# Kernel tuning notes

Hardware: AMD Instinct MI355X
Metric: run time of the kernel (lower is better)

## Reference

```python
import jax, jax.numpy as jnp
import numpy as np

KERNEL_MUL = 2.0
KERNEL_NUM = 5


def setup_inputs() -> dict:
    key = jax.random.key(0)
    k1, k2 = jax.random.split(key)
    source = jax.random.normal(k1, (4096, 256), dtype=jnp.float32)
    target = jax.random.normal(k2, (4096, 256), dtype=jnp.float32)
    return {"source": source, "target": target}


def _mmd(source, target):
    b = source.shape[0]
    total = jnp.concatenate([source, target], axis=0)  # [2N, D]
    n = total.shape[0]
    # pairwise squared L2 via gram trick (avoids O(N^2 * D) intermediate)
    sq = jnp.sum(total * total, axis=1)  # [2N]
    d2 = sq[:, None] + sq[None, :] - 2.0 * (total @ total.T)
    d2 = jnp.maximum(d2, 0.0)  # [2N, 2N]
    # bandwidth from detached distances (matches L2_distance.data)
    bandwidth = jax.lax.stop_gradient(jnp.sum(d2)) / (n * n - n)
    bandwidth = bandwidth / (KERNEL_MUL ** (KERNEL_NUM // 2))
    kernels = jnp.zeros_like(d2)
    for i in range(KERNEL_NUM):
        kernels = kernels + jnp.exp(-d2 / (bandwidth * KERNEL_MUL ** i))
    XX = kernels[:b, :b]
    YY = kernels[b:, b:]
    XY = kernels[:b, b:]
    YX = kernels[b:, :b]
    return jnp.mean(XX + YY - XY - YX)


def reference(source, target):
    return _mmd(source, target)
```

## Files before the change

kernel.cpp:

```cpp
#include <hip/hip_runtime.h>
#include <hip/hip_bf16.h>


#define N_TOTAL 8192
#define B_HALF 4096
#define D_DIM 256
#define TILE 128
#define NTILE 64
#define NTRI 2080

typedef float f32x16 __attribute__((ext_vector_type(16)));
typedef _Float16 f16x8 __attribute__((ext_vector_type(8)));

__device__ __forceinline__ const float* row_base(const float* src, const float* tgt, int r) {
    return (r < B_HALF) ? src + (size_t)r * D_DIM : tgt + (size_t)(r - B_HALF) * D_DIM;
}

__global__ __launch_bounds__(256) void prep_kernel(const float* __restrict__ src,
                                                   const float* __restrict__ tgt,
                                                   _Float16* __restrict__ a16f,
                                                   float* __restrict__ sq,
                                                   float* __restrict__ colpart) {
    int tid = threadIdx.x, w = tid >> 6, lane = tid & 63;
    int r0 = blockIdx.x * 128;
    #pragma unroll 4
    for (int i = 0; i < 32; ++i) {
        int row = r0 + w * 32 + i;
        const float* rp = row_base(src, tgt, row);
        float4 v = ((const float4*)rp)[lane];
        _Float16 h[4] = {(_Float16)v.x, (_Float16)v.y, (_Float16)v.z, (_Float16)v.w};
        size_t idx = ((size_t)(lane >> 1) * N_TOTAL + row) * 8 + (lane & 1) * 4;
        *(ushort4*)(a16f + idx) = *(ushort4*)h;
        float s = v.x*v.x + v.y*v.y + v.z*v.z + v.w*v.w;
        #pragma unroll
        for (int off = 32; off; off >>= 1) s += __shfl_down(s, off, 64);
        if (lane == 0) sq[row] = s;
    }
    float c = 0.f;
    for (int r = r0; r < r0 + 128; ++r)
        c += row_base(src, tgt, r)[tid];
    colpart[blockIdx.x * D_DIM + tid] = c;
}

__global__ __launch_bounds__(256) void bw_kernel(const float* __restrict__ sq,
                                                 const float* __restrict__ colpart,
                                                 float* __restrict__ negc,
                                                 double* __restrict__ accum) {
    __shared__ double red[256];
    int t = threadIdx.x;
    double s = 0.0;
    for (int i = t; i < N_TOTAL; i += 256) s += (double)sq[i];
    red[t] = s;
    __syncthreads();
    for (int off = 128; off; off >>= 1) {
        if (t < off) red[t] += red[t + off];
        __syncthreads();
    }
    double sumsq = red[0];
    __syncthreads();
    float c = 0.f;
    #pragma unroll
    for (int k = 0; k < 64; ++k) c += colpart[k * D_DIM + t];
    red[t] = (double)c * (double)c;
    __syncthreads();
    for (int off = 128; off; off >>= 1) {
        if (t < off) red[t] += red[t + off];
        __syncthreads();
    }
    if (t == 0) {
        double S1 = 2.0 * (double)N_TOTAL * sumsq - 2.0 * red[0];
        double nn = (double)N_TOTAL * (double)N_TOTAL - (double)N_TOTAL;
        double bw = S1 / nn / 4.0;
        negc[0] = (float)(-1.4426950408889634 / (16.0 * bw));
        accum[0] = 0.0;
    }
}

__global__ __launch_bounds__(256, 4) void mmd_main(const _Float16* __restrict__ a16f,
                                                   const float* __restrict__ sq,
                                                   const float* __restrict__ negc,
                                                   double* __restrict__ accum) {
    __shared__ float wsum[4];

    int b  = blockIdx.x;
    int bs = (b & 7) * (NTRI / 8) + (b >> 3);
    int it = 0, cum = 0;
    while (cum + (NTILE - it) <= bs) { cum += NTILE - it; ++it; }
    int jt = it + (bs - cum);

    int tid = threadIdx.x, lane = tid & 63, wid = tid >> 6;
    int wrow = wid >> 1, wcol = wid & 1;
    int rowA = it * TILE, rowB = jt * TILE;
    int c32 = lane & 31, khalf = lane >> 5;

    const _Float16* PA = a16f + (size_t)khalf * (N_TOTAL * 8)
                              + (size_t)(rowA + wrow * 64 + c32) * 8;
    const _Float16* PB = a16f + (size_t)khalf * (N_TOTAL * 8)
                              + (size_t)(rowB + wcol * 64 + c32) * 8;

    f32x16 acc[2][2] = {};

    #pragma unroll 4
    for (int kap = 0; kap < 16; ++kap) {
        size_t ko = (size_t)kap * (N_TOTAL * 16);
        f16x8 af[2], bf[2];
        af[0] = *(const f16x8*)(PA + ko);
        af[1] = *(const f16x8*)(PA + ko + 32 * 8);
        bf[0] = *(const f16x8*)(PB + ko);
        bf[1] = *(const f16x8*)(PB + ko + 32 * 8);
        #pragma unroll
        for (int mt = 0; mt < 2; ++mt)
            #pragma unroll
            for (int nt = 0; nt < 2; ++nt)
                acc[mt][nt] = __builtin_amdgcn_mfma_f32_32x32x16_f16(af[mt], bf[nt], acc[mt][nt], 0, 0, 0);
    }

    float nc = *negc;
    float sjn[2];
    #pragma unroll
    for (int nt = 0; nt < 2; ++nt)
        sjn[nt] = sq[rowB + wcol * 64 + nt * 32 + c32];
    float tsum = 0.f;
    #pragma unroll
    for (int mt = 0; mt < 2; ++mt) {
        #pragma unroll
        for (int reg = 0; reg < 16; ++reg) {
            int i = rowA + wrow * 64 + mt * 32 + (reg & 3) + 8 * (reg >> 2) + 4 * khalf;
            float si = sq[i];
            #pragma unroll
            for (int nt = 0; nt < 2; ++nt) {
                float d2 = fmaxf(si + sjn[nt] - 2.0f * acc[mt][nt][reg], 0.f);
                float u  = exp2f(nc * d2);
                float u2 = u * u, u4 = u2 * u2, u8 = u4 * u4;
                tsum += u + u2 + u4 + u8 + u8 * u8;
            }
        }
    }
    float scale = (((it < 32) == (jt < 32)) ? 1.f : -1.f) * ((it == jt) ? 1.f : 2.f);
    tsum *= scale;

    #pragma unroll
    for (int off = 32; off; off >>= 1) tsum += __shfl_down(tsum, off, 64);
    if (lane == 0) wsum[wid] = tsum;
    __syncthreads();
    if (tid == 0) {
        float t = wsum[0] + wsum[1] + wsum[2] + wsum[3];
        atomicAdd(accum, (double)t);
    }
}

__global__ void finalize_kernel(const double* __restrict__ accum, float* __restrict__ out) {
    out[0] = (float)(accum[0] / ((double)B_HALF * (double)B_HALF));
}

extern "C" void kernel_launch(void* const* d_in, const int* in_sizes, int n_in,
                              void* d_out, int out_size, void* d_ws, size_t ws_size,
                              hipStream_t stream) {
    const float* src = (const float*)d_in[0];
    const float* tgt = (const float*)d_in[1];
    float* out = (float*)d_out;

    char* ws = (char*)d_ws;
    float*  sq      = (float*)ws;
    float*  colpart = (float*)(ws + 32768);
    float*  negc    = (float*)(ws + 98304);
    double* accum   = (double*)(ws + 98312);
    _Float16* a16f  = (_Float16*)(ws + 131072);

    prep_kernel<<<64, 256, 0, stream>>>(src, tgt, a16f, sq, colpart);
    bw_kernel<<<1, 256, 0, stream>>>(sq, colpart, negc, accum);
    mmd_main<<<NTRI, 256, 0, stream>>>(a16f, sq, negc, accum);
    finalize_kernel<<<1, 1, 0, stream>>>(accum, out);
}
```

Measured before the change: 79.11 us.

## Stage A tile in LDS via direct global-to-LDS loads; widen prep kernel

```diff
diff --git a/kernel.cpp b/kernel.cpp
--- a/kernel.cpp
+++ b/kernel.cpp
@@ -22,24 +22,37 @@
                                                    float* __restrict__ sq,
                                                    float* __restrict__ colpart) {
     int tid = threadIdx.x, w = tid >> 6, lane = tid & 63;
-    int r0 = blockIdx.x * 128;
-    #pragma unroll 4
-    for (int i = 0; i < 32; ++i) {
-        int row = r0 + w * 32 + i;
+    int r0 = blockIdx.x * 32;
+
+    #pragma unroll
+    for (int i = 0; i < 8; ++i) {
+        int row = r0 + w * 8 + i;
         const float* rp = row_base(src, tgt, row);
         float4 v = ((const float4*)rp)[lane];
-        _Float16 h[4] = {(_Float16)v.x, (_Float16)v.y, (_Float16)v.z, (_Float16)v.w};
-        size_t idx = ((size_t)(lane >> 1) * N_TOTAL + row) * 8 + (lane & 1) * 4;
-        *(ushort4*)(a16f + idx) = *(ushort4*)h;
         float s = v.x*v.x + v.y*v.y + v.z*v.z + v.w*v.w;
         #pragma unroll
         for (int off = 32; off; off >>= 1) s += __shfl_down(s, off, 64);
         if (lane == 0) sq[row] = s;
     }
+
     float c = 0.f;
-    for (int r = r0; r < r0 + 128; ++r)
+    for (int r = r0; r < r0 + 32; ++r)
         c += row_base(src, tgt, r)[tid];
     colpart[blockIdx.x * D_DIM + tid] = c;
+
+    int wg = blockIdx.x * 4 + w;
+    #pragma unroll
+    for (int i = 0; i < 4; ++i) {
+        int t  = wg * 4 + i;
+        int kb = t >> 7, rg = t & 127;
+        int row = rg * 64 + lane;
+        const float* rp = row_base(src, tgt, row) + kb * 8;
+        float4 v0 = ((const float4*)rp)[0];
+        float4 v1 = ((const float4*)rp)[1];
+        _Float16 h[8] = {(_Float16)v0.x, (_Float16)v0.y, (_Float16)v0.z, (_Float16)v0.w,
+                         (_Float16)v1.x, (_Float16)v1.y, (_Float16)v1.z, (_Float16)v1.w};
+        *(f16x8*)(a16f + ((size_t)kb * N_TOTAL + row) * 8) = *(f16x8*)h;
+    }
 }
 
 __global__ __launch_bounds__(256) void bw_kernel(const float* __restrict__ sq,
@@ -59,8 +72,7 @@
     double sumsq = red[0];
     __syncthreads();
     float c = 0.f;
-    #pragma unroll
-    for (int k = 0; k < 64; ++k) c += colpart[k * D_DIM + t];
+    for (int k = 0; k < 256; ++k) c += colpart[k * D_DIM + t];
     red[t] = (double)c * (double)c;
     __syncthreads();
     for (int off = 128; off; off >>= 1) {
@@ -76,10 +88,17 @@
     }
 }
 
-__global__ __launch_bounds__(256, 4) void mmd_main(const _Float16* __restrict__ a16f,
+__device__ __forceinline__ void gload_lds16(const void* g, void* l) {
+    __builtin_amdgcn_global_load_lds((const __attribute__((address_space(1))) unsigned int*)g,
+                                     (__attribute__((address_space(3))) unsigned int*)l,
+                                     16, 0, 0);
+}
+
+__global__ __launch_bounds__(256, 2) void mmd_main(const _Float16* __restrict__ a16f,
                                                    const float* __restrict__ sq,
                                                    const float* __restrict__ negc,
                                                    double* __restrict__ accum) {
+    __shared__ _Float16 Asm[32 * TILE * 8];
     __shared__ float wsum[4];
 
     int b  = blockIdx.x;
@@ -93,19 +112,30 @@
     int rowA = it * TILE, rowB = jt * TILE;
     int c32 = lane & 31, khalf = lane >> 5;
 
-    const _Float16* PA = a16f + (size_t)khalf * (N_TOTAL * 8)
-                              + (size_t)(rowA + wrow * 64 + c32) * 8;
+    #pragma unroll
+    for (int i = 0; i < 16; ++i) {
+        int g0 = i * 256 + wid * 64;
+        int g  = g0 + lane;
+        int kb = g >> 7, r = g & 127;
+        gload_lds16(a16f + ((size_t)kb * N_TOTAL + rowA + r) * 8,
+                    Asm + (size_t)g0 * 8);
+    }
+
     const _Float16* PB = a16f + (size_t)khalf * (N_TOTAL * 8)
                               + (size_t)(rowB + wcol * 64 + c32) * 8;
 
+    asm volatile("s_waitcnt vmcnt(0)" ::: "memory");
+    __syncthreads();
+
     f32x16 acc[2][2] = {};
 
     #pragma unroll 4
     for (int kap = 0; kap < 16; ++kap) {
+        int kb = kap * 2 + khalf;
         size_t ko = (size_t)kap * (N_TOTAL * 16);
         f16x8 af[2], bf[2];
-        af[0] = *(const f16x8*)(PA + ko);
-        af[1] = *(const f16x8*)(PA + ko + 32 * 8);
+        af[0] = *(const f16x8*)&Asm[((size_t)kb * TILE + wrow * 64 + c32) * 8];
+        af[1] = *(const f16x8*)&Asm[((size_t)kb * TILE + wrow * 64 + 32 + c32) * 8];
         bf[0] = *(const f16x8*)(PB + ko);
         bf[1] = *(const f16x8*)(PB + ko + 32 * 8);
         #pragma unroll
@@ -163,11 +193,11 @@
     char* ws = (char*)d_ws;
     float*  sq      = (float*)ws;
     float*  colpart = (float*)(ws + 32768);
-    float*  negc    = (float*)(ws + 98304);
-    double* accum   = (double*)(ws + 98312);
-    _Float16* a16f  = (_Float16*)(ws + 131072);
-
-    prep_kernel<<<64, 256, 0, stream>>>(src, tgt, a16f, sq, colpart);
+    float*  negc    = (float*)(ws + 294912);
+    double* accum   = (double*)(ws + 294920);
+    _Float16* a16f  = (_Float16*)(ws + 327680);
+
+    prep_kernel<<<256, 256, 0, stream>>>(src, tgt, a16f, sq, colpart);
     bw_kernel<<<1, 256, 0, stream>>>(sq, colpart, negc, accum);
     mmd_main<<<NTRI, 256, 0, stream>>>(a16f, sq, negc, accum);
     finalize_kernel<<<1, 1, 0, stream>>>(accum, out);
```

Measured after the change: 79.04 us. Within noise of the previous version (-0.1%).
